# Kernel tuning notes

Measured on AMD Instinct MI355X. Metric: run time of the kernel, lower is better.

The kernel has to match this reference:

```python
import jax, jax.numpy as jnp
import numpy as np

B, IN, OUT = 4096, 1024, 1024

def setup_inputs() -> dict:
    key = jax.random.key(0)
    k1, k2 = jax.random.split(key)
    xs = jax.random.uniform(k1, (B, IN), dtype=jnp.float32)          # fuzzy truth values in [0,1]
    weights = jax.random.normal(k2, (IN, OUT), dtype=jnp.float32)    # raw weights (pre-sigmoid)
    return {"xs": xs, "weights": weights}


def reference(xs, weights):
    # get_weights(): sigmoid maps raw params to valid fuzzy booleans in [0,1]
    w = jax.nn.sigmoid(weights)                                       # [IN, OUT]
    # Weighted Lukasiewicz conjunction:
    #   out[b, j] = max(0, 1 - sum_i w[i, j] * (1 - xs[b, i]))
    # Broadcast+reduce collapses to a single GEMM over in_features.
    s = jnp.einsum('bi,io->bo', 1.0 - xs, w)                          # [B, OUT]
    return jnp.maximum(1.0 - s, 0.0)
```

## Files before the change

kernel.cpp:

```cpp
#include <hip/hip_runtime.h>
#include <hip/hip_bf16.h>
#include <math.h>


constexpr int Bsz = 4096;
constexpr int IN  = 1024;
constexpr int OUT = 1024;

constexpr int BM = 64;
constexpr int BN = 64;
constexpr int BK = 64;

typedef __attribute__((ext_vector_type(8))) short bf16x8;
typedef __attribute__((ext_vector_type(4))) float f32x4;

__device__ inline unsigned short f2bf(float f) {
    union { float f; unsigned u; } c{f};
    unsigned lsb = (c.u >> 16) & 1u;
    unsigned r = c.u + 0x7fffu + lsb;
    return (unsigned short)(r >> 16);
}

__global__ void prep_fused(const float* __restrict__ xs, const float* __restrict__ w,
                           unsigned short* __restrict__ A, unsigned short* __restrict__ WT) {
    if (blockIdx.x < 2048) {
        int idx = (blockIdx.x * 256 + threadIdx.x) * 2;
        float4 v0 = ((const float4*)xs)[idx];
        float4 v1 = ((const float4*)xs)[idx + 1];
        ushort4 o0, o1;
        o0.x = f2bf(1.0f - v0.x); o0.y = f2bf(1.0f - v0.y);
        o0.z = f2bf(1.0f - v0.z); o0.w = f2bf(1.0f - v0.w);
        o1.x = f2bf(1.0f - v1.x); o1.y = f2bf(1.0f - v1.y);
        o1.z = f2bf(1.0f - v1.z); o1.w = f2bf(1.0f - v1.w);
        ((ushort4*)A)[idx]     = o0;
        ((ushort4*)A)[idx + 1] = o1;
    } else {
        __shared__ unsigned short t[32][33];
        int wblk = blockIdx.x - 2048;
        int o0 = (wblk & 31) * 32, i0 = (wblk >> 5) * 32;
        int tx = threadIdx.x & 31, ty = threadIdx.x >> 5;
#pragma unroll
        for (int r = 0; r < 4; ++r) {
            int row = ty + r * 8;
            float v = w[(size_t)(i0 + row) * OUT + o0 + tx];
            float s = 1.0f / (1.0f + __expf(-v));
            t[row][tx] = f2bf(s);
        }
        __syncthreads();
#pragma unroll
        for (int r = 0; r < 4; ++r) {
            int row = ty + r * 8;
            WT[(size_t)(o0 + row) * IN + i0 + tx] = t[tx][row];
        }
    }
}

__global__ __launch_bounds__(256, 4) void gemm_fuzzy(const unsigned short* __restrict__ A,
                                                     const unsigned short* __restrict__ Bt,
                                                     float* __restrict__ C) {
    __shared__ unsigned short As[2][BM * BK];
    __shared__ unsigned short Bs[2][BN * BK];

    const int tid  = threadIdx.x;
    const int lane = tid & 63;
    const int wave = tid >> 6;
    const int quad = lane >> 4;
    const int l16  = lane & 15;
    const int wm   = (wave >> 1) * 32;
    const int wn   = (wave & 1) * 32;
    const int bm   = blockIdx.y * BM;
    const int bn   = blockIdx.x * BN;

    const int c0 = tid, c1 = tid + 256;
    const int ar0 = c0 >> 3, ak0 = c0 & 7;
    const int ar1 = c1 >> 3, ak1 = c1 & 7;
    const unsigned short* Ag0 = A  + (size_t)(bm + ar0) * IN + ak0 * 8;
    const unsigned short* Ag1 = A  + (size_t)(bm + ar1) * IN + ak1 * 8;
    const unsigned short* Bg0 = Bt + (size_t)(bn + ar0) * IN + ak0 * 8;
    const unsigned short* Bg1 = Bt + (size_t)(bn + ar1) * IN + ak1 * 8;
    const int ad0 = ((c0 & ~7) | (ak0 ^ (ar0 & 7))) * 8;
    const int ad1 = ((c1 & ~7) | (ak1 ^ (ar1 & 7))) * 8;

    bf16x8 rA[2][2], rB[2][2];

    rA[0][0] = *(const bf16x8*)Ag0; rA[0][1] = *(const bf16x8*)Ag1;
    rB[0][0] = *(const bf16x8*)Bg0; rB[0][1] = *(const bf16x8*)Bg1;
    *(bf16x8*)&As[0][ad0] = rA[0][0]; *(bf16x8*)&As[0][ad1] = rA[0][1];
    *(bf16x8*)&Bs[0][ad0] = rB[0][0]; *(bf16x8*)&Bs[0][ad1] = rB[0][1];
    rA[1][0] = *(const bf16x8*)(Ag0 + BK); rA[1][1] = *(const bf16x8*)(Ag1 + BK);
    rB[1][0] = *(const bf16x8*)(Bg0 + BK); rB[1][1] = *(const bf16x8*)(Bg1 + BK);
    __syncthreads();

    f32x4 acc[2][2] = {};
    const int NIT = IN / BK;

#pragma unroll
    for (int i = 0; i < NIT; ++i) {
        if (i + 2 < NIT) {
            int k0 = (i + 2) * BK;
            rA[i & 1][0] = *(const bf16x8*)(Ag0 + k0);
            rA[i & 1][1] = *(const bf16x8*)(Ag1 + k0);
            rB[i & 1][0] = *(const bf16x8*)(Bg0 + k0);
            rB[i & 1][1] = *(const bf16x8*)(Bg1 + k0);
        }

        const unsigned short* as = As[i & 1];
        const unsigned short* bs = Bs[i & 1];
#pragma unroll
        for (int s = 0; s < 2; ++s) {
            const int kc = s * 4 + quad;
            bf16x8 af[2], bfr[2];
#pragma unroll
            for (int mt = 0; mt < 2; ++mt) {
                int row = wm + mt * 16 + l16;
                af[mt] = *(const bf16x8*)&as[(row * 8 + (kc ^ (row & 7))) * 8];
            }
#pragma unroll
            for (int nt = 0; nt < 2; ++nt) {
                int row = wn + nt * 16 + l16;
                bfr[nt] = *(const bf16x8*)&bs[(row * 8 + (kc ^ (row & 7))) * 8];
            }
#pragma unroll
            for (int mt = 0; mt < 2; ++mt)
#pragma unroll
                for (int nt = 0; nt < 2; ++nt)
                    acc[mt][nt] = __builtin_amdgcn_mfma_f32_16x16x32_bf16(
                        af[mt], bfr[nt], acc[mt][nt], 0, 0, 0);
        }

        if (i + 1 < NIT) {
            int nb = (i + 1) & 1;
            *(bf16x8*)&As[nb][ad0] = rA[nb][0]; *(bf16x8*)&As[nb][ad1] = rA[nb][1];
            *(bf16x8*)&Bs[nb][ad0] = rB[nb][0]; *(bf16x8*)&Bs[nb][ad1] = rB[nb][1];
        }
        __syncthreads();
    }

#pragma unroll
    for (int mt = 0; mt < 2; ++mt) {
#pragma unroll
        for (int nt = 0; nt < 2; ++nt) {
#pragma unroll
            for (int r = 0; r < 4; ++r) {
                int row = bm + wm + mt * 16 + quad * 4 + r;
                int col = bn + wn + nt * 16 + l16;
                float v = 1.0f - acc[mt][nt][r];
                C[(size_t)row * OUT + col] = fmaxf(v, 0.0f);
            }
        }
    }
}

extern "C" void kernel_launch(void* const* d_in, const int* in_sizes, int n_in,
                              void* d_out, int out_size, void* d_ws, size_t ws_size,
                              hipStream_t stream) {
    const float* xs = (const float*)d_in[0];
    const float* wt = (const float*)d_in[1];
    float* out = (float*)d_out;

    unsigned short* A  = (unsigned short*)d_ws;
    unsigned short* WT = (unsigned short*)((char*)d_ws + (size_t)Bsz * IN * 2);

    prep_fused<<<2048 + 1024, 256, 0, stream>>>(xs, wt, A, WT);
    gemm_fuzzy<<<dim3(OUT / BN, Bsz / BM), 256, 0, stream>>>(A, WT, out);
}
```

Measured before the change: 88.38 us.

## Enlarge GEMM tiles to 128x128 with 64x64 per-wave subtiles

```diff
diff --git a/kernel.cpp b/kernel.cpp
--- a/kernel.cpp
+++ b/kernel.cpp
@@ -7,8 +7,8 @@
 constexpr int IN  = 1024;
 constexpr int OUT = 1024;
 
-constexpr int BM = 64;
-constexpr int BN = 64;
+constexpr int BM = 128;
+constexpr int BN = 128;
 constexpr int BK = 64;
 
 typedef __attribute__((ext_vector_type(8))) short bf16x8;
@@ -55,7 +55,7 @@
     }
 }
 
-__global__ __launch_bounds__(256, 4) void gemm_fuzzy(const unsigned short* __restrict__ A,
+__global__ __launch_bounds__(256, 1) void gemm_fuzzy(const unsigned short* __restrict__ A,
                                                      const unsigned short* __restrict__ Bt,
                                                      float* __restrict__ C) {
     __shared__ unsigned short As[2][BM * BK];
@@ -66,42 +66,49 @@
     const int wave = tid >> 6;
     const int quad = lane >> 4;
     const int l16  = lane & 15;
-    const int wm   = (wave >> 1) * 32;
-    const int wn   = (wave & 1) * 32;
-    const int bm   = blockIdx.y * BM;
-    const int bn   = blockIdx.x * BN;
+    const int wm   = (wave >> 1) * 64;
+    const int wn   = (wave & 1) * 64;
+    const int bm   = (blockIdx.x >> 3) * BM;
+    const int bn   = (blockIdx.x & 7) * BN;
 
-    const int c0 = tid, c1 = tid + 256;
-    const int ar0 = c0 >> 3, ak0 = c0 & 7;
-    const int ar1 = c1 >> 3, ak1 = c1 & 7;
-    const unsigned short* Ag0 = A  + (size_t)(bm + ar0) * IN + ak0 * 8;
-    const unsigned short* Ag1 = A  + (size_t)(bm + ar1) * IN + ak1 * 8;
-    const unsigned short* Bg0 = Bt + (size_t)(bn + ar0) * IN + ak0 * 8;
-    const unsigned short* Bg1 = Bt + (size_t)(bn + ar1) * IN + ak1 * 8;
-    const int ad0 = ((c0 & ~7) | (ak0 ^ (ar0 & 7))) * 8;
-    const int ad1 = ((c1 & ~7) | (ak1 ^ (ar1 & 7))) * 8;
+    int arow[4], adst[4];
+    const unsigned short* Ag[4];
+    const unsigned short* Bg[4];
+#pragma unroll
+    for (int r = 0; r < 4; ++r) {
+        int c = tid + r * 256;
+        int row = c >> 3, kc = c & 7;
+        arow[r] = row;
+        adst[r] = (row * 8 + (kc ^ (row & 7))) * 8;
+        Ag[r] = A  + (size_t)(bm + row) * IN + kc * 8;
+        Bg[r] = Bt + (size_t)(bn + row) * IN + kc * 8;
+    }
 
-    bf16x8 rA[2][2], rB[2][2];
+    bf16x8 rA[2][4], rB[2][4];
 
-    rA[0][0] = *(const bf16x8*)Ag0; rA[0][1] = *(const bf16x8*)Ag1;
-    rB[0][0] = *(const bf16x8*)Bg0; rB[0][1] = *(const bf16x8*)Bg1;
-    *(bf16x8*)&As[0][ad0] = rA[0][0]; *(bf16x8*)&As[0][ad1] = rA[0][1];
-    *(bf16x8*)&Bs[0][ad0] = rB[0][0]; *(bf16x8*)&Bs[0][ad1] = rB[0][1];
-    rA[1][0] = *(const bf16x8*)(Ag0 + BK); rA[1][1] = *(const bf16x8*)(Ag1 + BK);
-    rB[1][0] = *(const bf16x8*)(Bg0 + BK); rB[1][1] = *(const bf16x8*)(Bg1 + BK);
+#pragma unroll
+    for (int r = 0; r < 4; ++r) { rA[0][r] = *(const bf16x8*)Ag[r]; rB[0][r] = *(const bf16x8*)Bg[r]; }
+#pragma unroll
+    for (int r = 0; r < 4; ++r) {
+        *(bf16x8*)&As[0][adst[r]] = rA[0][r];
+        *(bf16x8*)&Bs[0][adst[r]] = rB[0][r];
+    }
+#pragma unroll
+    for (int r = 0; r < 4; ++r) { rA[1][r] = *(const bf16x8*)(Ag[r] + BK); rB[1][r] = *(const bf16x8*)(Bg[r] + BK); }
     __syncthreads();
 
-    f32x4 acc[2][2] = {};
+    f32x4 acc[4][4] = {};
     const int NIT = IN / BK;
 
 #pragma unroll
     for (int i = 0; i < NIT; ++i) {
         if (i + 2 < NIT) {
             int k0 = (i + 2) * BK;
-            rA[i & 1][0] = *(const bf16x8*)(Ag0 + k0);
-            rA[i & 1][1] = *(const bf16x8*)(Ag1 + k0);
-            rB[i & 1][0] = *(const bf16x8*)(Bg0 + k0);
-            rB[i & 1][1] = *(const bf16x8*)(Bg1 + k0);
+#pragma unroll
+            for (int r = 0; r < 4; ++r) {
+                rA[i & 1][r] = *(const bf16x8*)(Ag[r] + k0);
+                rB[i & 1][r] = *(const bf16x8*)(Bg[r] + k0);
+            }
         }
 
         const unsigned short* as = As[i & 1];
@@ -109,37 +116,40 @@
 #pragma unroll
         for (int s = 0; s < 2; ++s) {
             const int kc = s * 4 + quad;
-            bf16x8 af[2], bfr[2];
+            bf16x8 af[4], bfr[4];
 #pragma unroll
-            for (int mt = 0; mt < 2; ++mt) {
+            for (int mt = 0; mt < 4; ++mt) {
                 int row = wm + mt * 16 + l16;
                 af[mt] = *(const bf16x8*)&as[(row * 8 + (kc ^ (row & 7))) * 8];
             }
 #pragma unroll
-            for (int nt = 0; nt < 2; ++nt) {
+            for (int nt = 0; nt < 4; ++nt) {
                 int row = wn + nt * 16 + l16;
                 bfr[nt] = *(const bf16x8*)&bs[(row * 8 + (kc ^ (row & 7))) * 8];
             }
 #pragma unroll
-            for (int mt = 0; mt < 2; ++mt)
+            for (int mt = 0; mt < 4; ++mt)
 #pragma unroll
-                for (int nt = 0; nt < 2; ++nt)
+                for (int nt = 0; nt < 4; ++nt)
                     acc[mt][nt] = __builtin_amdgcn_mfma_f32_16x16x32_bf16(
                         af[mt], bfr[nt], acc[mt][nt], 0, 0, 0);
         }
 
         if (i + 1 < NIT) {
             int nb = (i + 1) & 1;
-            *(bf16x8*)&As[nb][ad0] = rA[nb][0]; *(bf16x8*)&As[nb][ad1] = rA[nb][1];
-            *(bf16x8*)&Bs[nb][ad0] = rB[nb][0]; *(bf16x8*)&Bs[nb][ad1] = rB[nb][1];
+#pragma unroll
+            for (int r = 0; r < 4; ++r) {
+                *(bf16x8*)&As[nb][adst[r]] = rA[nb][r];
+                *(bf16x8*)&Bs[nb][adst[r]] = rB[nb][r];
+            }
         }
         __syncthreads();
     }
 
 #pragma unroll
-    for (int mt = 0; mt < 2; ++mt) {
+    for (int mt = 0; mt < 4; ++mt) {
 #pragma unroll
-        for (int nt = 0; nt < 2; ++nt) {
+        for (int nt = 0; nt < 4; ++nt) {
 #pragma unroll
             for (int r = 0; r < 4; ++r) {
                 int row = bm + wm + mt * 16 + quad * 4 + r;
@@ -162,5 +172,5 @@
     unsigned short* WT = (unsigned short*)((char*)d_ws + (size_t)Bsz * IN * 2);
 
     prep_fused<<<2048 + 1024, 256, 0, stream>>>(xs, wt, A, WT);
-    gemm_fuzzy<<<dim3(OUT / BN, Bsz / BM), 256, 0, stream>>>(A, WT, out);
+    gemm_fuzzy<<<256, 256, 0, stream>>>(A, WT, out);
 }
```

Result: no change. 87.97 us (-0.5%).
